# Performance work log

Measured on AMD Instinct MI355X. Metric: run time of the kernel, lower is better.

## Reference

```python
import jax, jax.numpy as jnp
import numpy as np

N = 100000
E = 1600000
IN_C = 256
OUT_C = 128


def setup_inputs() -> dict:
    key = jax.random.key(0)
    ks = jax.random.split(key, 8)
    x = jax.random.normal(ks[0], (N, IN_C), dtype=jnp.float32)
    edge_index = jax.random.randint(ks[1], (2, E), 0, N, dtype=jnp.int64)
    # GCNConv params (weight + bias)
    W = jax.random.normal(ks[2], (IN_C, OUT_C), dtype=jnp.float32) / np.sqrt(IN_C)
    b = jnp.zeros((OUT_C,), dtype=jnp.float32)
    # residual Linear params
    Wr = jax.random.normal(ks[3], (IN_C, OUT_C), dtype=jnp.float32) / np.sqrt(IN_C)
    br = jnp.zeros((OUT_C,), dtype=jnp.float32)
    # LayerNorm params
    gamma = jnp.ones((OUT_C,), dtype=jnp.float32)
    beta = jnp.zeros((OUT_C,), dtype=jnp.float32)
    return {"x": x, "edge_index": edge_index, "W": W, "b": b,
            "Wr": Wr, "br": br, "gamma": gamma, "beta": beta}


def _gcn_conv(x, src, dst, W, b):
    # PyG GCNConv: add self-loops, symmetric degree normalization,
    # transform first (out < in), then gather-scale-scatter.
    n = x.shape[0]
    loops = jnp.arange(n, dtype=src.dtype)
    src = jnp.concatenate([src, loops])
    dst = jnp.concatenate([dst, loops])
    ones = jnp.ones_like(dst, dtype=x.dtype)
    deg = jax.ops.segment_sum(ones, dst, num_segments=n)  # [N]
    dinv = jnp.where(deg > 0, jax.lax.rsqrt(deg), 0.0)
    norm = dinv[src] * dinv[dst]                           # [E+N]
    h = x @ W                                              # [N, out]
    msg = h[src] * norm[:, None]                           # [E+N, out]
    agg = jax.ops.segment_sum(msg, dst, num_segments=n)    # [N, out]
    return agg + b


def _layer_norm(x, gamma, beta, eps=1e-5):
    mu = jnp.mean(x, axis=-1, keepdims=True)
    var = jnp.mean(jnp.square(x - mu), axis=-1, keepdims=True)
    return (x - mu) * jax.lax.rsqrt(var + eps) * gamma + beta


def reference(x, edge_index, W, b, Wr, br, gamma, beta):
    src, dst = edge_index[0], edge_index[1]
    res = x @ Wr + br
    h = _gcn_conv(x, src, dst, W, b)
    out = _layer_norm(h + res, gamma, beta)
    return jax.nn.relu(out)
```

## Files before the change

kernel.cpp:

```cpp
#include <hip/hip_runtime.h>
#include <hip/hip_fp8.h>

typedef __attribute__((ext_vector_type(8))) short bf16x8;
typedef __attribute__((ext_vector_type(4))) float f32x4;
typedef __attribute__((ext_vector_type(8))) unsigned short ushort8;
typedef __attribute__((ext_vector_type(4))) unsigned short ushort4v;

__device__ __forceinline__ unsigned short f2bf(float f) {
  unsigned int u = __float_as_uint(f);
  u = u + 0x7FFFu + ((u >> 16) & 1u);
  return (unsigned short)(u >> 16);
}

__device__ __forceinline__ unsigned char ftofp8(float f) {
  __hip_fp8_e4m3 t(f);
  return (unsigned char)t.__x;
}
__device__ __forceinline__ float2 fp8x2tof(unsigned short u) {
  __hip_fp8_e4m3 a, b;
  a.__x = (unsigned char)(u & 0xFF);
  b.__x = (unsigned char)(u >> 8);
  return make_float2((float)a, (float)b);
}

#define GLOAD_LDS16(g, l)                                                            \
  __builtin_amdgcn_global_load_lds((const __attribute__((address_space(1))) void*)(g), \
                                   (__attribute__((address_space(3))) void*)(l), 16, 0, 0)

__global__ void k_pre(const float* __restrict__ W, const float* __restrict__ Wr,
                      unsigned short* __restrict__ Wb,
                      const int* __restrict__ dst, int* __restrict__ deg,
                      int* __restrict__ slot, int E) {
  if (blockIdx.x < 8) {
    int t = blockIdx.x * 256 + threadIdx.x;
    int col = t >> 3, g = t & 7;
    const float* Ws = (col < 128) ? (W + col) : (Wr + (col - 128));
#pragma unroll
    for (int kt = 0; kt < 4; ++kt) {
      ushort8 u;
#pragma unroll
      for (int j = 0; j < 8; ++j) u[j] = f2bf(Ws[(size_t)(kt * 64 + g * 8 + j) * 128]);
      *(ushort8*)&Wb[kt * 16384 + col * 64 + ((g ^ (col & 7)) * 8)] = u;
    }
    return;
  }
  int base = ((blockIdx.x - 8) * 256 + threadIdx.x) * 4;
  if (base + 3 < E) {
    int4 d = *(const int4*)(dst + base);
    int r0 = atomicAdd(&deg[d.x], 1);
    int r1 = atomicAdd(&deg[d.y], 1);
    int r2 = atomicAdd(&deg[d.z], 1);
    int r3 = atomicAdd(&deg[d.w], 1);
    int4 s = make_int4(r0 < 64 ? d.x * 64 + r0 : -1, r1 < 64 ? d.y * 64 + r1 : -1,
                       r2 < 64 ? d.z * 64 + r2 : -1, r3 < 64 ? d.w * 64 + r3 : -1);
    *(int4*)(slot + base) = s;
  } else {
    for (int e = base; e < E; ++e) {
      int d = dst[e];
      int r = atomicAdd(&deg[d], 1);
      slot[e] = (r < 64) ? d * 64 + r : -1;
    }
  }
}

__global__ __launch_bounds__(512) void k_gemm(
    const float* __restrict__ x, const unsigned short* __restrict__ Wb,
    const float* __restrict__ br, const int* __restrict__ deg,
    unsigned char* __restrict__ hs8, float* res, int N,
    const int* __restrict__ src, const int* __restrict__ slot,
    int* __restrict__ ssrc, int E)
{
  __shared__ unsigned short xt[128 * 64];
  __shared__ unsigned short wt[256 * 64];
  int tid = threadIdx.x;
  int lane = tid & 63, w = tid >> 6;
  int lo = lane & 15, hi = lane >> 4;
  int brow = blockIdx.x * 128;

  f32x4 acc[16];
#pragma unroll
  for (int c = 0; c < 16; ++c) acc[c] = (f32x4){0.f, 0.f, 0.f, 0.f};

  for (int kt = 0; kt < 4; ++kt) {
    int k0 = kt * 64;
    const unsigned short* gw = Wb + kt * 16384;
#pragma unroll
    for (int i = 0; i < 4; ++i) {
      int off = i * 4096 + tid * 8;
      GLOAD_LDS16(gw + off, &wt[off]);
    }
#pragma unroll
    for (int r = 0; r < 4; ++r) {
      int idx = tid + 512 * r;
      int row = idx >> 4, kq = idx & 15;
      int node = brow + row;
      float4 v = make_float4(0.f, 0.f, 0.f, 0.f);
      if (node < N) v = *(const float4*)(x + (size_t)node * 256 + k0 + kq * 4);
      ushort4v u;
      u[0] = f2bf(v.x); u[1] = f2bf(v.y); u[2] = f2bf(v.z); u[3] = f2bf(v.w);
      int g = kq >> 1, h = kq & 1;
      *(ushort4v*)(&xt[row * 64 + ((g ^ (row & 7)) * 8) + h * 4]) = u;
    }
    __syncthreads();
#pragma unroll
    for (int kk = 0; kk < 2; ++kk) {
      int row = w * 16 + lo;
      int gsel = kk * 4 + hi;
      bf16x8 a = *(const bf16x8*)(&xt[row * 64 + ((gsel ^ (row & 7)) * 8)]);
      int gsw = (gsel ^ (lo & 7)) * 8;
#pragma unroll
      for (int c = 0; c < 16; ++c) {
        bf16x8 b = *(const bf16x8*)(&wt[(c * 16 + lo) * 64 + gsw]);
        acc[c] = __builtin_amdgcn_mfma_f32_16x16x32_bf16(a, b, acc[c], 0, 0, 0);
      }
    }
    __syncthreads();
  }
  float di4[4];
#pragma unroll
  for (int rg = 0; rg < 4; ++rg) {
    int row = brow + w * 16 + hi * 4 + rg;
    di4[rg] = (row < N) ? rsqrtf((float)(deg[row] + 1)) : 0.f;
  }
#pragma unroll
  for (int c = 0; c < 16; ++c) {
    int colo = c * 16 + lo;
#pragma unroll
    for (int rg = 0; rg < 4; ++rg) {
      int row = brow + w * 16 + hi * 4 + rg;
      if (row < N) {
        float v = acc[c][rg];
        if (colo < 128) hs8[(size_t)row * 128 + colo] = ftofp8(v * di4[rg]);
        else            res[(size_t)row * 128 + (colo - 128)] = v + br[colo - 128];
      }
    }
  }

  int ebase = blockIdx.x * 2048 + tid * 4;
  if (ebase + 3 < E) {
    int4 t = *(const int4*)(slot + ebase);
    int4 s = *(const int4*)(src + ebase);
    if (t.x >= 0) ssrc[t.x] = s.x;
    if (t.y >= 0) ssrc[t.y] = s.y;
    if (t.z >= 0) ssrc[t.z] = s.z;
    if (t.w >= 0) ssrc[t.w] = s.w;
  } else {
    for (int e = ebase; e < E; ++e) {
      int t = slot[e];
      if (t >= 0) ssrc[t] = src[e];
    }
  }
}

__global__ __launch_bounds__(256) void k_agg(
    const unsigned short* __restrict__ hsu, const float* resin,
    const int* __restrict__ deg, const int* __restrict__ ssrc,
    const float* __restrict__ bias, const float* __restrict__ gamma,
    const float* __restrict__ beta, float* out, int N)
{
  int node = blockIdx.x * 4 + (threadIdx.x >> 6);
  int lane = threadIdx.x & 63;
  if (node >= N) return;
  float2 sf = fp8x2tof(hsu[(size_t)node * 64 + lane]);
  float ax = sf.x, ay = sf.y;
  int cnt = deg[node];
  float di = rsqrtf((float)(cnt + 1));
  if (cnt > 64) cnt = 64;
  const int* sp = ssrc + (size_t)node * 64;
  int e = 0;
  for (; e + 16 <= cnt; e += 16) {
    int idx[16];
#pragma unroll
    for (int j = 0; j < 16; ++j) idx[j] = sp[e + j];
    unsigned short u[16];
#pragma unroll
    for (int j = 0; j < 16; ++j) u[j] = hsu[(size_t)idx[j] * 64 + lane];
    float sx = 0.f, sy = 0.f;
#pragma unroll
    for (int j = 0; j < 16; ++j) { float2 d = fp8x2tof(u[j]); sx += d.x; sy += d.y; }
    ax += sx; ay += sy;
  }
  for (; e + 4 <= cnt; e += 4) {
    int i0 = sp[e + 0], i1 = sp[e + 1], i2 = sp[e + 2], i3 = sp[e + 3];
    unsigned short u0 = hsu[(size_t)i0 * 64 + lane];
    unsigned short u1 = hsu[(size_t)i1 * 64 + lane];
    unsigned short u2 = hsu[(size_t)i2 * 64 + lane];
    unsigned short u3 = hsu[(size_t)i3 * 64 + lane];
    float2 d0 = fp8x2tof(u0), d1 = fp8x2tof(u1), d2 = fp8x2tof(u2), d3 = fp8x2tof(u3);
    ax += (d0.x + d1.x) + (d2.x + d3.x);
    ay += (d0.y + d1.y) + (d2.y + d3.y);
  }
  for (; e < cnt; ++e) {
    float2 d = fp8x2tof(hsu[(size_t)sp[e] * 64 + lane]);
    ax += d.x; ay += d.y;
  }
  float2 r  = ((const float2*)resin)[(size_t)node * 64 + lane];
  float2 bb = ((const float2*)bias)[lane];
  float vx = ax * di + bb.x + r.x;
  float vy = ay * di + bb.y + r.y;
  float sum = vx + vy;
#pragma unroll
  for (int off = 32; off >= 1; off >>= 1) sum += __shfl_xor(sum, off, 64);
  float mean = sum * (1.0f / 128.0f);
  float dx = vx - mean, dy = vy - mean;
  float sq = dx * dx + dy * dy;
#pragma unroll
  for (int off = 32; off >= 1; off >>= 1) sq += __shfl_xor(sq, off, 64);
  float rstd = rsqrtf(sq * (1.0f / 128.0f) + 1e-5f);
  float2 g  = ((const float2*)gamma)[lane];
  float2 be = ((const float2*)beta)[lane];
  float ox = fmaxf(dx * rstd * g.x + be.x, 0.0f);
  float oy = fmaxf(dy * rstd * g.y + be.y, 0.0f);
  ((float2*)out)[(size_t)node * 64 + lane] = make_float2(ox, oy);
}

extern "C" void kernel_launch(void* const* d_in, const int* in_sizes, int n_in,
                              void* d_out, int out_size, void* d_ws, size_t ws_size,
                              hipStream_t stream) {
  const float* x     = (const float*)d_in[0];
  const int*   eidx  = (const int*)d_in[1];
  const float* W     = (const float*)d_in[2];
  const float* b     = (const float*)d_in[3];
  const float* Wr    = (const float*)d_in[4];
  const float* br    = (const float*)d_in[5];
  const float* gamma = (const float*)d_in[6];
  const float* beta  = (const float*)d_in[7];
  float* out = (float*)d_out;

  int N = in_sizes[0] / 256;
  int E = in_sizes[1] / 2;
  const int* srcI = eidx;
  const int* dstI = eidx + E;

  char* w = (char*)d_ws;
  size_t off = 0;
  auto alloc = [&](size_t bytes) -> void* {
    void* p = w + off;
    off += (bytes + 255) & ~(size_t)255;
    return p;
  };
  unsigned char* hs8 = (unsigned char*)alloc((size_t)N * 128);
  int*   deg    = (int*)alloc((size_t)N * 4);
  int*   slot   = (int*)alloc((size_t)E * 4);
  int*   ssrc   = (int*)alloc((size_t)N * 64 * 4);
  unsigned short* Wb = (unsigned short*)alloc((size_t)4 * 16384 * 2);

  hipMemsetAsync(deg, 0, (size_t)N * 4, stream);
  int dgrid = (E / 4 + 255) / 256;
  k_pre <<<8 + dgrid, 256, 0, stream>>>(W, Wr, Wb, dstI, deg, slot, E);
  int ggrid = (N + 127) / 128;
  k_gemm<<<ggrid, 512, 0, stream>>>(x, Wb, br, deg, hs8, out, N, srcI, slot, ssrc, E);
  k_agg <<<(N + 3) / 4, 256, 0, stream>>>((const unsigned short*)hs8, out, deg, ssrc,
                                          b, gamma, beta, out, N);
}
```

Before: 199.2 us.

## Pre-convert x to swizzled bf16 tiles in k_pre and stream them via LDS loads

Adds a phase in the preprocessing kernel that converts x to bf16 in the swizzled per-tile layout the GEMM expects. The GEMM then loads both operands directly into LDS with async global_load_lds and does no in-kernel fp32 conversion. This removes register-path loads and conversion work from the GEMM, at the cost of an extra bf16 write and read of x through memory. A fallback keeps the old GEMM when the workspace is too small.

```diff
diff --git a/kernel.cpp b/kernel.cpp
--- a/kernel.cpp
+++ b/kernel.cpp
@@ -29,8 +29,9 @@
 
 __global__ void k_pre(const float* __restrict__ W, const float* __restrict__ Wr,
                       unsigned short* __restrict__ Wb,
+                      const float* __restrict__ x, unsigned short* __restrict__ xb, int CV,
                       const int* __restrict__ dst, int* __restrict__ deg,
-                      int* __restrict__ slot, int E) {
+                      int* __restrict__ slot, int E, int N) {
   if (blockIdx.x < 8) {
     int t = blockIdx.x * 256 + threadIdx.x;
     int col = t >> 3, g = t & 7;
@@ -44,7 +45,29 @@
     }
     return;
   }
-  int base = ((blockIdx.x - 8) * 256 + threadIdx.x) * 4;
+  if ((int)blockIdx.x < 8 + CV) {
+    int b = blockIdx.x - 8;
+    int tid = threadIdx.x;
+#pragma unroll
+    for (int t = 0; t < 16; ++t) {
+      int gid = t * 256 + tid;
+      int kt = gid >> 10, q = gid & 1023;
+      int row = q >> 3, gsw = q & 7;
+      int g = gsw ^ (row & 7);
+      int node = b * 128 + row;
+      ushort8 u = (ushort8){0, 0, 0, 0, 0, 0, 0, 0};
+      if (node < N) {
+        const float* xr = x + (size_t)node * 256 + kt * 64 + g * 8;
+        float4 v0 = *(const float4*)xr;
+        float4 v1 = *(const float4*)(xr + 4);
+        u[0] = f2bf(v0.x); u[1] = f2bf(v0.y); u[2] = f2bf(v0.z); u[3] = f2bf(v0.w);
+        u[4] = f2bf(v1.x); u[5] = f2bf(v1.y); u[6] = f2bf(v1.z); u[7] = f2bf(v1.w);
+      }
+      *(ushort8*)&xb[((size_t)b * 4 + kt) * 8192 + (size_t)q * 8] = u;
+    }
+    return;
+  }
+  int base = ((blockIdx.x - 8 - CV) * 256 + threadIdx.x) * 4;
   if (base + 3 < E) {
     int4 d = *(const int4*)(dst + base);
     int r0 = atomicAdd(&deg[d.x], 1);
@@ -64,6 +87,89 @@
 }
 
 __global__ __launch_bounds__(512) void k_gemm(
+    const float* __restrict__ x, const unsigned short* __restrict__ Wb,
+    const unsigned short* __restrict__ xb,
+    const float* __restrict__ br, const int* __restrict__ deg,
+    unsigned char* __restrict__ hs8, float* res, int N,
+    const int* __restrict__ src, const int* __restrict__ slot,
+    int* __restrict__ ssrc, int E)
+{
+  __shared__ unsigned short xt[128 * 64];
+  __shared__ unsigned short wt[256 * 64];
+  int tid = threadIdx.x;
+  int lane = tid & 63, w = tid >> 6;
+  int lo = lane & 15, hi = lane >> 4;
+  int brow = blockIdx.x * 128;
+
+  f32x4 acc[16];
+#pragma unroll
+  for (int c = 0; c < 16; ++c) acc[c] = (f32x4){0.f, 0.f, 0.f, 0.f};
+
+  for (int kt = 0; kt < 4; ++kt) {
+    const unsigned short* gw = Wb + kt * 16384;
+#pragma unroll
+    for (int i = 0; i < 4; ++i) {
+      int off = i * 4096 + tid * 8;
+      GLOAD_LDS16(gw + off, &wt[off]);
+    }
+    const unsigned short* gx = xb + ((size_t)blockIdx.x * 4 + kt) * 8192;
+#pragma unroll
+    for (int i = 0; i < 2; ++i) {
+      int off = i * 4096 + tid * 8;
+      GLOAD_LDS16(gx + off, &xt[off]);
+    }
+    __syncthreads();
+#pragma unroll
+    for (int kk = 0; kk < 2; ++kk) {
+      int row = w * 16 + lo;
+      int gsel = kk * 4 + hi;
+      bf16x8 a = *(const bf16x8*)(&xt[row * 64 + ((gsel ^ (row & 7)) * 8)]);
+      int gsw = (gsel ^ (lo & 7)) * 8;
+#pragma unroll
+      for (int c = 0; c < 16; ++c) {
+        bf16x8 b = *(const bf16x8*)(&wt[(c * 16 + lo) * 64 + gsw]);
+        acc[c] = __builtin_amdgcn_mfma_f32_16x16x32_bf16(a, b, acc[c], 0, 0, 0);
+      }
+    }
+    __syncthreads();
+  }
+  float di4[4];
+#pragma unroll
+  for (int rg = 0; rg < 4; ++rg) {
+    int row = brow + w * 16 + hi * 4 + rg;
+    di4[rg] = (row < N) ? rsqrtf((float)(deg[row] + 1)) : 0.f;
+  }
+#pragma unroll
+  for (int c = 0; c < 16; ++c) {
+    int colo = c * 16 + lo;
+#pragma unroll
+    for (int rg = 0; rg < 4; ++rg) {
+      int row = brow + w * 16 + hi * 4 + rg;
+      if (row < N) {
+        float v = acc[c][rg];
+        if (colo < 128) hs8[(size_t)row * 128 + colo] = ftofp8(v * di4[rg]);
+        else            res[(size_t)row * 128 + (colo - 128)] = v + br[colo - 128];
+      }
+    }
+  }
+
+  int ebase = blockIdx.x * 2048 + tid * 4;
+  if (ebase + 3 < E) {
+    int4 t = *(const int4*)(slot + ebase);
+    int4 s = *(const int4*)(src + ebase);
+    if (t.x >= 0) ssrc[t.x] = s.x;
+    if (t.y >= 0) ssrc[t.y] = s.y;
+    if (t.z >= 0) ssrc[t.z] = s.z;
+    if (t.w >= 0) ssrc[t.w] = s.w;
+  } else {
+    for (int e = ebase; e < E; ++e) {
+      int t = slot[e];
+      if (t >= 0) ssrc[t] = src[e];
+    }
+  }
+}
+
+__global__ __launch_bounds__(512) void k_gemm_fb(
     const float* __restrict__ x, const unsigned short* __restrict__ Wb,
     const float* __restrict__ br, const int* __restrict__ deg,
     unsigned char* __restrict__ hs8, float* res, int N,
@@ -245,11 +351,18 @@
   int*   ssrc   = (int*)alloc((size_t)N * 64 * 4);
   unsigned short* Wb = (unsigned short*)alloc((size_t)4 * 16384 * 2);
 
+  int ggrid = (N + 127) / 128;
+  size_t xb_bytes = (size_t)ggrid * 4 * 8192 * 2;
+  int CV = (ws_size >= off + ((xb_bytes + 255) & ~(size_t)255)) ? ggrid : 0;
+  unsigned short* xb = CV ? (unsigned short*)alloc(xb_bytes) : nullptr;
+
   hipMemsetAsync(deg, 0, (size_t)N * 4, stream);
   int dgrid = (E / 4 + 255) / 256;
-  k_pre <<<8 + dgrid, 256, 0, stream>>>(W, Wr, Wb, dstI, deg, slot, E);
-  int ggrid = (N + 127) / 128;
-  k_gemm<<<ggrid, 512, 0, stream>>>(x, Wb, br, deg, hs8, out, N, srcI, slot, ssrc, E);
+  k_pre <<<8 + CV + dgrid, 256, 0, stream>>>(W, Wr, Wb, x, xb, CV, dstI, deg, slot, E, N);
+  if (CV)
+    k_gemm<<<ggrid, 512, 0, stream>>>(x, Wb, xb, br, deg, hs8, out, N, srcI, slot, ssrc, E);
+  else
+    k_gemm_fb<<<ggrid, 512, 0, stream>>>(x, Wb, br, deg, hs8, out, N, srcI, slot, ssrc, E);
   k_agg <<<(N + 3) / 4, 256, 0, stream>>>((const unsigned short*)hs8, out, deg, ssrc,
                                           b, gamma, beta, out, N);
 }
```

Result: slower. 206.8 us (+3.8%).
